# Optimization experiments

Hardware: AMD Instinct MI355X
Metric: run time of the kernel (lower is better)

The kernel has to match this reference:

```python
import jax, jax.numpy as jnp
import numpy as np

MASK_VALUE = -1e6  # d2l.sequence_mask fills with -1000000.0, not -inf


def setup_inputs() -> dict:
    key = jax.random.key(0)
    kq, kk, kv, kl = jax.random.split(key, 4)
    B, Lq, Lk, D = 8, 2048, 2048, 128
    queries = jax.random.normal(kq, (B, Lq, D), dtype=jnp.float32)
    keys = jax.random.normal(kk, (B, Lk, D), dtype=jnp.float32)
    values = jax.random.normal(kv, (B, Lk, D), dtype=jnp.float32)
    valid_lens = jax.random.randint(kl, (B,), 1, Lk + 1, dtype=jnp.int32)
    return {"queries": queries, "keys": keys, "values": values, "valid_lens": valid_lens}


def reference(queries, keys, values, valid_lens):
    # scores: [B, Lq, Lk]
    d = queries.shape[-1]
    scale = 1.0 / np.sqrt(d).astype(np.float32)
    scores = jnp.einsum('bqd,bkd->bqk', queries, keys) * scale
    # 1D valid_lens -> same mask for every query row of a batch element
    mask = jnp.arange(keys.shape[1]) < valid_lens[:, None, None]  # [B,1,Lk]
    scores = jnp.where(mask, scores, MASK_VALUE)
    attn = jax.nn.softmax(scores, axis=-1)
    # dropout p=0.0 -> identity
    return jnp.einsum('bqk,bkd->bqd', attn, values)
```

## Files before the change

kernel.cpp:

```cpp
#include <hip/hip_runtime.h>
#include <hip/hip_bf16.h>

typedef __attribute__((ext_vector_type(8))) short short8;
typedef __attribute__((ext_vector_type(4))) short short4v;
typedef __attribute__((ext_vector_type(4))) float f32x4;

#define LQ     2048
#define LK     2048
#define DH     128
#define NB     8
#define KBLK   64
#define SPLITW 512
#define NSMAX  4
#define NQT64  (LQ / 64)

#define QBF_OFF (0ull)
#define KBF_OFF (4ull << 20)
#define VT_OFF  (8ull << 20)
#define OP_OFF  (12ull << 20)
#define ML_OFF  (76ull << 20)

static __device__ __forceinline__ unsigned short f2bf(float f) {
  __hip_bfloat16 h = __float2bfloat16(f);
  return __builtin_bit_cast(unsigned short, h);
}

#define GLDS16(gp, lp) __builtin_amdgcn_global_load_lds(                    \
    (const __attribute__((address_space(1))) void*)(gp),                    \
    (__attribute__((address_space(3))) void*)(lp), 16, 0, 0)

__global__ void __launch_bounds__(256)
prep_qk(const float* __restrict__ Qg, const float* __restrict__ Kg,
        unsigned short* __restrict__ Qbf, unsigned short* __restrict__ Kbf) {
  const float SCALE = 0.08838834764831845f * 1.4426950408889634f;
  const int NQE8 = NB * LQ * DH / 8;
  int g = blockIdx.x * 256 + threadIdx.x;
  const float* src;
  unsigned short* dst;
  float sc;
  int off;
  if (g < NQE8) { src = Qg; dst = Qbf; sc = SCALE; off = g * 8; }
  else          { src = Kg; dst = Kbf; sc = 1.0f;  off = (g - NQE8) * 8; }
  float4 a = *(const float4*)(src + off);
  float4 b = *(const float4*)(src + off + 4);
  short8 v;
  v[0] = (short)f2bf(a.x * sc); v[1] = (short)f2bf(a.y * sc);
  v[2] = (short)f2bf(a.z * sc); v[3] = (short)f2bf(a.w * sc);
  v[4] = (short)f2bf(b.x * sc); v[5] = (short)f2bf(b.y * sc);
  v[6] = (short)f2bf(b.z * sc); v[7] = (short)f2bf(b.w * sc);
  *(short8*)(dst + off) = v;
}

__global__ void __launch_bounds__(256)
prep_vt(const float* __restrict__ Vg, unsigned short* __restrict__ Vt) {
  __shared__ unsigned short Lt[64][68];
  int bid = blockIdx.x;
  int dt = bid & 1;
  int kt = (bid >> 1) & 31;
  int b  = bid >> 6;
  int t  = threadIdx.x;
  int kr = t >> 2, dc = (t & 3) * 16;
  const float* vp = Vg + (((size_t)b * LK + kt * 64 + kr) * DH + dt * 64 + dc);
#pragma unroll
  for (int j = 0; j < 4; ++j) {
    float4 x = *(const float4*)(vp + j * 4);
    Lt[kr][dc + j * 4 + 0] = f2bf(x.x);
    Lt[kr][dc + j * 4 + 1] = f2bf(x.y);
    Lt[kr][dc + j * 4 + 2] = f2bf(x.z);
    Lt[kr][dc + j * 4 + 3] = f2bf(x.w);
  }
  __syncthreads();
  int dr = t >> 2, kc = (t & 3) * 16;
  short8 w0, w1;
#pragma unroll
  for (int j = 0; j < 8; ++j) w0[j] = (short)Lt[kc + j][dr];
#pragma unroll
  for (int j = 0; j < 8; ++j) w1[j] = (short)Lt[kc + 8 + j][dr];
  unsigned short* op = Vt + (((size_t)b * DH + dt * 64 + dr) * LK + kt * 64 + kc);
  *(short8*)op = w0;
  *(short8*)(op + 8) = w1;
}

__global__ void __launch_bounds__(256, 2)
attn_split(const unsigned short* __restrict__ Qbf, const unsigned short* __restrict__ Kbf,
           const unsigned short* __restrict__ Vt, const int* __restrict__ vlens,
           float* __restrict__ Opart, float* __restrict__ Ml) {
  const int bid   = blockIdx.x;
  const int qt    = bid & (NQT64 - 1);
  const int split = (bid >> 5) & (NSMAX - 1);
  const int b     = bid >> 7;

  const int vlen = vlens[b];
  const int kbeg = split * SPLITW;
  if (kbeg >= vlen) return;
  const int kend  = min(vlen, kbeg + SPLITW);
  const int ntile = (kend - kbeg + KBLK - 1) / KBLK;

  const int tid  = threadIdx.x;
  const int lane = tid & 63;
  const int w    = tid >> 6;
  const int l15  = lane & 15;
  const int lg   = lane >> 4;

  __shared__ __align__(16) unsigned char Kl[2][16384];
  __shared__ __align__(16) unsigned char Vl[2][16384];
  __shared__ __align__(16) unsigned char Pw[4][2048];

  const int qrow = qt * 64 + w * 16 + l15;
  const unsigned short* qp = Qbf + ((size_t)(b * LQ + qrow)) * DH;
  short8 qf[4];
#pragma unroll
  for (int dk = 0; dk < 4; ++dk) qf[dk] = *(const short8*)(qp + dk * 32 + lg * 8);

  f32x4 o[8];
#pragma unroll
  for (int i = 0; i < 8; ++i) o[i] = (f32x4){0.f, 0.f, 0.f, 0.f};
  float rm = -1e30f;
  float rl = 0.f;

  const char* Kbase = (const char*)(Kbf + (size_t)b * LK * DH);
  const char* Vbase = (const char*)(Vt + (size_t)b * DH * LK);

#define STAGE(t, bsel) do {                                                  \
    const int t0s = kbeg + (t) * KBLK;                                       \
    const char* kg_ = Kbase + (size_t)t0s * (DH * 2);                        \
    _Pragma("unroll")                                                        \
    for (int j = 0; j < 4; ++j) {                                            \
      unsigned ko_ = (unsigned)(w * 4096 + j * 1024 + lane * 16);            \
      unsigned ks_ = ko_ ^ (((ko_ >> 8) & 7u) << 4);                         \
      GLDS16(kg_ + ks_, &Kl[bsel][w * 4096 + j * 1024]);                     \
    }                                                                        \
    _Pragma("unroll")                                                        \
    for (int j = 0; j < 4; ++j) {                                            \
      unsigned vo_ = (unsigned)(w * 4096 + j * 1024 + lane * 16);            \
      unsigned d_  = vo_ >> 7;                                               \
      unsigned vs_ = (vo_ & 127u) ^ ((d_ & 7u) << 4);                        \
      const char* vg_ = Vbase + ((size_t)d_ * LK + t0s) * 2 + vs_;           \
      GLDS16(vg_, &Vl[bsel][w * 4096 + j * 1024]);                           \
    }                                                                        \
  } while (0)

  int cur = 0;
  STAGE(0, 0);
  __syncthreads();

  for (int tt = 0; tt < ntile; ++tt) {
    const int t0 = kbeg + tt * KBLK;
    if (tt + 1 < ntile) STAGE(tt + 1, cur ^ 1);

    const unsigned char* Kb = Kl[cur];
    const unsigned char* Vb = Vl[cur];

    f32x4 s[4];
#pragma unroll
    for (int ks = 0; ks < 4; ++ks) {
      f32x4 acc = (f32x4){0.f, 0.f, 0.f, 0.f};
      const int krow = ks * 16 + l15;
      const unsigned swzk = ((unsigned)(krow & 7)) << 4;
#pragma unroll
      for (int dk = 0; dk < 4; ++dk) {
        unsigned off = ((unsigned)(krow * 256 + dk * 64 + lg * 16)) ^ swzk;
        short8 kf = *(const short8*)(Kb + off);
        acc = __builtin_amdgcn_mfma_f32_16x16x32_bf16(kf, qf[dk], acc, 0, 0, 0);
      }
      s[ks] = acc;
    }

    if (t0 + KBLK > kend) {
#pragma unroll
      for (int ks = 0; ks < 4; ++ks) {
#pragma unroll
        for (int r = 0; r < 4; ++r) {
          if (t0 + ks * 16 + lg * 4 + r >= kend) s[ks][r] = -1e30f;
        }
      }
    }

    float mk[4];
#pragma unroll
    for (int ks = 0; ks < 4; ++ks)
      mk[ks] = fmaxf(fmaxf(s[ks][0], s[ks][1]), fmaxf(s[ks][2], s[ks][3]));
    float tm = fmaxf(fmaxf(mk[0], mk[1]), fmaxf(mk[2], mk[3]));
    tm = fmaxf(tm, __shfl_xor(tm, 16));
    tm = fmaxf(tm, __shfl_xor(tm, 32));
    float nm = fmaxf(rm, tm);
    float corr = exp2f(rm - nm);
    rm = nm;
#pragma unroll
    for (int ks = 0; ks < 4; ++ks) {
#pragma unroll
      for (int r = 0; r < 4; ++r) s[ks][r] = exp2f(s[ks][r] - nm);
    }

#pragma unroll
    for (int ks = 0; ks < 4; ++ks) {
      short4v wv;
      wv[0] = (short)f2bf(s[ks][0]); wv[1] = (short)f2bf(s[ks][1]);
      wv[2] = (short)f2bf(s[ks][2]); wv[3] = (short)f2bf(s[ks][3]);
      unsigned off = (unsigned)(l15 * 128 + ks * 32 + lg * 8) ^ ((unsigned)(l15 & 7) << 4);
      *(short4v*)(Pw[w] + off) = wv;
    }

#pragma unroll
    for (int dc = 0; dc < 8; ++dc) o[dc] *= corr;
    float ts = ((s[0][0] + s[0][1]) + (s[0][2] + s[0][3]))
             + ((s[1][0] + s[1][1]) + (s[1][2] + s[1][3]))
             + ((s[2][0] + s[2][1]) + (s[2][2] + s[2][3]))
             + ((s[3][0] + s[3][1]) + (s[3][2] + s[3][3]));
    ts += __shfl_xor(ts, 16);
    ts += __shfl_xor(ts, 32);
    rl = rl * corr + ts;

    short8 pa[2];
#pragma unroll
    for (int kk = 0; kk < 2; ++kk) {
      unsigned off = (unsigned)(l15 * 128 + kk * 64 + lg * 16) ^ ((unsigned)(l15 & 7) << 4);
      pa[kk] = *(const short8*)(Pw[w] + off);
    }

#pragma unroll
    for (int dc = 0; dc < 8; ++dc) {
      const int d = dc * 16 + l15;
      const unsigned swzv = ((unsigned)(d & 7)) << 4;
#pragma unroll
      for (int kk = 0; kk < 2; ++kk) {
        unsigned off = ((unsigned)(d * 128 + kk * 64 + lg * 16)) ^ swzv;
        short8 vf = *(const short8*)(Vb + off);
        o[dc] = __builtin_amdgcn_mfma_f32_16x16x32_bf16(vf, pa[kk], o[dc], 0, 0, 0);
      }
    }

    __syncthreads();
    cur ^= 1;
  }

  float* op0 = Opart + ((size_t)(split * NB + b) * LQ + qt * 64 + w * 16) * DH;
#pragma unroll
  for (int dc = 0; dc < 8; ++dc) {
    *(f32x4*)(op0 + (size_t)l15 * DH + dc * 16 + lg * 4) = o[dc];
  }
  if (lane < 16) {
    size_t ro = (size_t)(split * NB + b) * LQ + qt * 64 + w * 16 + lane;
    float2 ml;
    ml.x = rm;
    ml.y = rl;
    *(float2*)(Ml + ro * 2) = ml;
  }
#undef STAGE
}

__global__ void __launch_bounds__(128)
attn_combine(const float* __restrict__ Opart, const float* __restrict__ Ml,
             const int* __restrict__ vlens, float* __restrict__ Og) {
  const int bid = blockIdx.x;
  const int b = bid >> 11;
  const int q = bid & (LQ - 1);
  const int d = threadIdx.x;
  const int nlive = (vlens[b] + SPLITW - 1) / SPLITW;
  float m = -1e30f;
  for (int s = 0; s < nlive; ++s)
    m = fmaxf(m, Ml[((size_t)(s * NB + b) * LQ + q) * 2]);
  float L = 0.f, acc = 0.f;
  for (int s = 0; s < nlive; ++s) {
    size_t ro = (size_t)(s * NB + b) * LQ + q;
    float w = exp2f(Ml[ro * 2] - m);
    L += w * Ml[ro * 2 + 1];
    acc += w * Opart[ro * DH + d];
  }
  Og[((size_t)b * LQ + q) * DH + d] = acc / L;
}

extern "C" void kernel_launch(void* const* d_in, const int* in_sizes, int n_in,
                              void* d_out, int out_size, void* d_ws, size_t ws_size,
                              hipStream_t stream) {
  const float* Q  = (const float*)d_in[0];
  const float* K  = (const float*)d_in[1];
  const float* V  = (const float*)d_in[2];
  const int*   vl = (const int*)d_in[3];
  float* O = (float*)d_out;

  unsigned short* Qbf = (unsigned short*)((char*)d_ws + QBF_OFF);
  unsigned short* Kbf = (unsigned short*)((char*)d_ws + KBF_OFF);
  unsigned short* Vt  = (unsigned short*)((char*)d_ws + VT_OFF);
  float* Opart = (float*)((char*)d_ws + OP_OFF);
  float* Ml    = (float*)((char*)d_ws + ML_OFF);

  hipLaunchKernelGGL(prep_qk, dim3(2048), dim3(256), 0, stream, Q, K, Qbf, Kbf);
  hipLaunchKernelGGL(prep_vt, dim3(512), dim3(256), 0, stream, V, Vt);
  hipLaunchKernelGGL(attn_split, dim3(NB * NSMAX * NQT64), dim3(256), 0, stream,
                     Qbf, Kbf, Vt, vl, Opart, Ml);
  hipLaunchKernelGGL(attn_combine, dim3(NB * LQ), dim3(128), 0, stream,
                     Opart, Ml, vl, O);
}
```

Baseline: 52.64 us.

## Store split partials in fp16, merge prep kernels, widen combine blocks

```diff
diff --git a/kernel.cpp b/kernel.cpp
--- a/kernel.cpp
+++ b/kernel.cpp
@@ -1,5 +1,6 @@
 #include <hip/hip_runtime.h>
 #include <hip/hip_bf16.h>
+#include <hip/hip_fp16.h>
 
 typedef __attribute__((ext_vector_type(8))) short short8;
 typedef __attribute__((ext_vector_type(4))) short short4v;
@@ -24,40 +25,46 @@
   __hip_bfloat16 h = __float2bfloat16(f);
   return __builtin_bit_cast(unsigned short, h);
 }
+static __device__ __forceinline__ short f2h(float f) {
+  __half h = __float2half(f);
+  return (short)__builtin_bit_cast(unsigned short, h);
+}
 
 #define GLDS16(gp, lp) __builtin_amdgcn_global_load_lds(                    \
     (const __attribute__((address_space(1))) void*)(gp),                    \
     (__attribute__((address_space(3))) void*)(lp), 16, 0, 0)
 
 __global__ void __launch_bounds__(256)
-prep_qk(const float* __restrict__ Qg, const float* __restrict__ Kg,
-        unsigned short* __restrict__ Qbf, unsigned short* __restrict__ Kbf) {
-  const float SCALE = 0.08838834764831845f * 1.4426950408889634f;
-  const int NQE8 = NB * LQ * DH / 8;
-  int g = blockIdx.x * 256 + threadIdx.x;
-  const float* src;
-  unsigned short* dst;
-  float sc;
-  int off;
-  if (g < NQE8) { src = Qg; dst = Qbf; sc = SCALE; off = g * 8; }
-  else          { src = Kg; dst = Kbf; sc = 1.0f;  off = (g - NQE8) * 8; }
-  float4 a = *(const float4*)(src + off);
-  float4 b = *(const float4*)(src + off + 4);
-  short8 v;
-  v[0] = (short)f2bf(a.x * sc); v[1] = (short)f2bf(a.y * sc);
-  v[2] = (short)f2bf(a.z * sc); v[3] = (short)f2bf(a.w * sc);
-  v[4] = (short)f2bf(b.x * sc); v[5] = (short)f2bf(b.y * sc);
-  v[6] = (short)f2bf(b.z * sc); v[7] = (short)f2bf(b.w * sc);
-  *(short8*)(dst + off) = v;
-}
-
-__global__ void __launch_bounds__(256)
-prep_vt(const float* __restrict__ Vg, unsigned short* __restrict__ Vt) {
+prep_all(const float* __restrict__ Qg, const float* __restrict__ Kg,
+         const float* __restrict__ Vg,
+         unsigned short* __restrict__ Qbf, unsigned short* __restrict__ Kbf,
+         unsigned short* __restrict__ Vt) {
   __shared__ unsigned short Lt[64][68];
-  int bid = blockIdx.x;
-  int dt = bid & 1;
-  int kt = (bid >> 1) & 31;
-  int b  = bid >> 6;
+  const int bid = blockIdx.x;
+  if (bid < 2048) {
+    const float SCALE = 0.08838834764831845f * 1.4426950408889634f;
+    const int NQE8 = NB * LQ * DH / 8;
+    int g = bid * 256 + threadIdx.x;
+    const float* src;
+    unsigned short* dst;
+    float sc;
+    int off;
+    if (g < NQE8) { src = Qg; dst = Qbf; sc = SCALE; off = g * 8; }
+    else          { src = Kg; dst = Kbf; sc = 1.0f;  off = (g - NQE8) * 8; }
+    float4 a = *(const float4*)(src + off);
+    float4 b = *(const float4*)(src + off + 4);
+    short8 v;
+    v[0] = (short)f2bf(a.x * sc); v[1] = (short)f2bf(a.y * sc);
+    v[2] = (short)f2bf(a.z * sc); v[3] = (short)f2bf(a.w * sc);
+    v[4] = (short)f2bf(b.x * sc); v[5] = (short)f2bf(b.y * sc);
+    v[6] = (short)f2bf(b.z * sc); v[7] = (short)f2bf(b.w * sc);
+    *(short8*)(dst + off) = v;
+    return;
+  }
+  int vb = bid - 2048;
+  int dt = vb & 1;
+  int kt = (vb >> 1) & 31;
+  int b  = vb >> 6;
   int t  = threadIdx.x;
   int kr = t >> 2, dc = (t & 3) * 16;
   const float* vp = Vg + (((size_t)b * LK + kt * 64 + kr) * DH + dt * 64 + dc);
@@ -84,7 +91,7 @@
 __global__ void __launch_bounds__(256, 2)
 attn_split(const unsigned short* __restrict__ Qbf, const unsigned short* __restrict__ Kbf,
            const unsigned short* __restrict__ Vt, const int* __restrict__ vlens,
-           float* __restrict__ Opart, float* __restrict__ Ml) {
+           __half* __restrict__ Opart, float* __restrict__ Ml) {
   const int bid   = blockIdx.x;
   const int qt    = bid & (NQT64 - 1);
   const int split = (bid >> 5) & (NSMAX - 1);
@@ -234,10 +241,13 @@
     cur ^= 1;
   }
 
-  float* op0 = Opart + ((size_t)(split * NB + b) * LQ + qt * 64 + w * 16) * DH;
+  __half* op0 = Opart + ((size_t)(split * NB + b) * LQ + qt * 64 + w * 16) * DH;
 #pragma unroll
   for (int dc = 0; dc < 8; ++dc) {
-    *(f32x4*)(op0 + (size_t)l15 * DH + dc * 16 + lg * 4) = o[dc];
+    short4v hv;
+    hv[0] = f2h(o[dc][0]); hv[1] = f2h(o[dc][1]);
+    hv[2] = f2h(o[dc][2]); hv[3] = f2h(o[dc][3]);
+    *(short4v*)(op0 + (size_t)l15 * DH + dc * 16 + lg * 4) = hv;
   }
   if (lane < 16) {
     size_t ro = (size_t)(split * NB + b) * LQ + qt * 64 + w * 16 + lane;
@@ -249,13 +259,14 @@
 #undef STAGE
 }
 
-__global__ void __launch_bounds__(128)
-attn_combine(const float* __restrict__ Opart, const float* __restrict__ Ml,
+__global__ void __launch_bounds__(256)
+attn_combine(const __half* __restrict__ Opart, const float* __restrict__ Ml,
              const int* __restrict__ vlens, float* __restrict__ Og) {
   const int bid = blockIdx.x;
-  const int b = bid >> 11;
-  const int q = bid & (LQ - 1);
-  const int d = threadIdx.x;
+  const int q0  = bid * 2;
+  const int b   = q0 >> 11;
+  const int q   = (q0 & (LQ - 1)) + (threadIdx.x >> 7);
+  const int d   = threadIdx.x & 127;
   const int nlive = (vlens[b] + SPLITW - 1) / SPLITW;
   float m = -1e30f;
   for (int s = 0; s < nlive; ++s)
@@ -265,7 +276,7 @@
     size_t ro = (size_t)(s * NB + b) * LQ + q;
     float w = exp2f(Ml[ro * 2] - m);
     L += w * Ml[ro * 2 + 1];
-    acc += w * Opart[ro * DH + d];
+    acc += w * __half2float(Opart[ro * DH + d]);
   }
   Og[((size_t)b * LQ + q) * DH + d] = acc / L;
 }
@@ -282,13 +293,12 @@
   unsigned short* Qbf = (unsigned short*)((char*)d_ws + QBF_OFF);
   unsigned short* Kbf = (unsigned short*)((char*)d_ws + KBF_OFF);
   unsigned short* Vt  = (unsigned short*)((char*)d_ws + VT_OFF);
-  float* Opart = (float*)((char*)d_ws + OP_OFF);
-  float* Ml    = (float*)((char*)d_ws + ML_OFF);
-
-  hipLaunchKernelGGL(prep_qk, dim3(2048), dim3(256), 0, stream, Q, K, Qbf, Kbf);
-  hipLaunchKernelGGL(prep_vt, dim3(512), dim3(256), 0, stream, V, Vt);
+  __half* Opart = (__half*)((char*)d_ws + OP_OFF);
+  float* Ml     = (float*)((char*)d_ws + ML_OFF);
+
+  hipLaunchKernelGGL(prep_all, dim3(2560), dim3(256), 0, stream, Q, K, V, Qbf, Kbf, Vt);
   hipLaunchKernelGGL(attn_split, dim3(NB * NSMAX * NQT64), dim3(256), 0, stream,
                      Qbf, Kbf, Vt, vl, Opart, Ml);
-  hipLaunchKernelGGL(attn_combine, dim3(NB * LQ), dim3(128), 0, stream,
+  hipLaunchKernelGGL(attn_combine, dim3(NB * LQ / 2), dim3(256), 0, stream,
                      Opart, Ml, vl, O);
 }
```

Measured after the change: 50.44 us. 1.04x faster.
